# Kernel tuning notes

Hardware: AMD Instinct MI355X
Metric: run time of the kernel (lower is better)

## Reference

```python
import jax, jax.numpy as jnp
import numpy as np

B, T, D, H, S = 4, 1024, 512, 8, 16
HD = D // H
PRUNING_THRESHOLD = 0.001


def setup_inputs() -> dict:
    key = jax.random.key(0)
    ks = jax.random.split(key, 7)
    x = jax.random.normal(ks[0], (B, T, D), jnp.float32)
    qkv_w = jax.random.normal(ks[1], (3 * D, D), jnp.float32) * (1.0 / np.sqrt(D))
    out_w = jax.random.normal(ks[2], (D, D), jnp.float32) * (1.0 / np.sqrt(D))
    # diverse-ish init for centers (exact init pattern doesn't affect the math being tested)
    base_centers = jax.random.normal(ks[3], (H, S, HD), jnp.float32) * 0.3
    center_deltas = jnp.zeros((H, S, HD), jnp.float32)
    log_scales = jax.random.normal(ks[4], (H, S), jnp.float32) * 0.5 - 0.5
    log_amps = jax.random.normal(ks[5], (H, S), jnp.float32) * 1.0 - 1.5
    movement_param = jnp.asarray(0.05, jnp.float32)
    temperature = jnp.ones((1,), jnp.float32)
    return {
        "x": x, "qkv_w": qkv_w, "out_w": out_w,
        "base_centers": base_centers, "center_deltas": center_deltas,
        "log_scales": log_scales, "log_amps": log_amps,
        "movement_param": movement_param, "temperature": temperature,
    }


def reference(x, qkv_w, out_w, base_centers, center_deltas, log_scales, log_amps,
              movement_param, temperature):
    Bx, Tx, Dx = x.shape
    Hh, Ss, hd = base_centers.shape

    # qkv projection (torch Linear, no bias: y = x @ W.T)
    qkv = (x @ qkv_w.T).reshape(Bx, Tx, 3, Hh, hd)
    q, k, v = qkv[:, :, 0], qkv[:, :, 1], qkv[:, :, 2]  # [B,T,H,hd]

    # effective centers with bounded movement
    move = jax.nn.sigmoid(movement_param) * 0.2
    centers = base_centers + center_deltas * move  # [H,S,hd]

    scales = jnp.clip(jnp.exp(log_scales), 1e-4, 5.0)       # [H,S]
    amps = jnp.clip(jnp.exp(log_amps), 1e-6, 10.0)          # [H,S]
    eff_amps = amps * (amps > PRUNING_THRESHOLD).astype(amps.dtype)
    inv_var = 1.0 / (scales ** 2 + 1e-8)                     # [H,S]

    # squared distances to splat centers: [B,T,H,S]
    q_d2 = jnp.minimum(jnp.sum((q[:, :, :, None, :] - centers[None, None]) ** 2, axis=-1), 100.0)
    k_d2 = jnp.minimum(jnp.sum((k[:, :, :, None, :] - centers[None, None]) ** 2, axis=-1), 100.0)

    q_w = jnp.exp(-0.5 * q_d2 * inv_var) * eff_amps  # [B,T,H,S]
    k_w = jnp.exp(-0.5 * k_d2 * inv_var) * eff_amps  # [B,T,H,S]

    # amplitude-weighted RBF scores: [B,T,T,H]
    logits = jnp.einsum('bihs,bjhs->bijh', q_w, k_w)

    temp = jnp.clip(temperature, 0.01, 10.0)[0]
    attn = jax.nn.softmax(logits / temp + 1e-8, axis=2)  # softmax over j

    out = jnp.einsum('bijh,bjhd->bihd', attn, v).reshape(Bx, Tx, Dx)
    out = out @ out_w.T
    return (out, attn)
```

## Files before the change

### kernel.cpp

```cpp
#include <hip/hip_runtime.h>
#include <hip/hip_bf16.h>

#define B_ 4
#define T_ 1024
#define D_ 512
#define H_ 8
#define S_ 16
#define HD_ 64
#define ITS 8
#define ITW 8
#define PVI 32
#define PVJ 64

typedef short bf16x8 __attribute__((ext_vector_type(8)));
typedef float f32x4m __attribute__((ext_vector_type(4)));

__device__ __forceinline__ unsigned short f2bf(float f) {
  unsigned u = __float_as_uint(f);
  unsigned r = (u + 0x7FFFu + ((u >> 16) & 1u)) >> 16;
  return (unsigned short)r;
}
__device__ __forceinline__ float bf2f(unsigned short h) {
  return __uint_as_float((unsigned)h << 16);
}

__device__ __forceinline__ void split4(const float4 v, ushort4& h, ushort4& l) {
  h.x = f2bf(v.x); l.x = f2bf(v.x - bf2f(h.x));
  h.y = f2bf(v.y); l.y = f2bf(v.y - bf2f(h.y));
  h.z = f2bf(v.z); l.z = f2bf(v.z - bf2f(h.z));
  h.w = f2bf(v.w); l.w = f2bf(v.w - bf2f(h.w));
}

__global__ void k_params(const float* __restrict__ base_centers,
                         const float* __restrict__ center_deltas,
                         const float* __restrict__ log_scales,
                         const float* __restrict__ log_amps,
                         const float* __restrict__ movement_param,
                         const float* __restrict__ temperature,
                         float* __restrict__ centers,
                         float* __restrict__ inv_var,
                         float* __restrict__ eff_amps,
                         float* __restrict__ inv_temp) {
  int tid = blockIdx.x * blockDim.x + threadIdx.x;
  float move = (1.f / (1.f + __expf(-movement_param[0]))) * 0.2f;
  if (tid < H_ * S_ * HD_)
    centers[tid] = base_centers[tid] + center_deltas[tid] * move;
  if (tid < H_ * S_) {
    float sc = __expf(log_scales[tid]);
    sc = fminf(fmaxf(sc, 1e-4f), 5.f);
    float am = __expf(log_amps[tid]);
    am = fminf(fmaxf(am, 1e-6f), 10.f);
    inv_var[tid] = 1.f / (sc * sc + 1e-8f);
    eff_amps[tid] = (am > 0.001f) ? am : 0.f;
  }
  if (tid == 0) {
    float t = fminf(fmaxf(temperature[0], 0.01f), 10.f);
    inv_temp[0] = 1.f / t;
  }
}

template <int BN>
__global__ __launch_bounds__(256) void gemm_mfma(const float* __restrict__ A,
                                                 const float* __restrict__ Bw,
                                                 float* __restrict__ C,
                                                 int M, int N, int K) {
  static_assert(BN == 64, "staging sized for BN=64");
  constexpr int NF = BN / 16;
  const int t = threadIdx.x;
  const int lane = t & 63;
  const int wv = t >> 6;
  const int mBase = blockIdx.y * 128;
  const int n0 = blockIdx.x * BN;
  const int lr = lane & 15;
  const int kg = lane >> 4;

  __shared__ unsigned short Ash[128][64];
  __shared__ unsigned short Asl[128][64];
  __shared__ unsigned short Bsh[64][64];
  __shared__ unsigned short Bsl[64][64];

  f32x4m acc[2][NF];
#pragma unroll
  for (int i = 0; i < 2; ++i)
#pragma unroll
    for (int f = 0; f < NF; ++f) {
      f32x4m z = {0.f, 0.f, 0.f, 0.f};
      acc[i][f] = z;
    }

  for (int k0 = 0; k0 < K; k0 += 64) {
    if (k0) __syncthreads();
#pragma unroll
    for (int r2 = 0; r2 < 2; ++r2) {
      int idx = t + r2 * 256;
      int row = idx >> 3, c8 = idx & 7;
      int c8s = c8 ^ (row & 7);
      const float* src = Bw + (size_t)(n0 + row) * K + k0 + c8 * 8;
      float4 v0 = *(const float4*)(src);
      float4 v1 = *(const float4*)(src + 4);
      ushort4 h0, l0, h1, l1;
      split4(v0, h0, l0); split4(v1, h1, l1);
      *(ushort4*)&Bsh[row][c8s * 8]     = h0;
      *(ushort4*)&Bsh[row][c8s * 8 + 4] = h1;
      *(ushort4*)&Bsl[row][c8s * 8]     = l0;
      *(ushort4*)&Bsl[row][c8s * 8 + 4] = l1;
    }
#pragma unroll
    for (int r4 = 0; r4 < 4; ++r4) {
      int idx = t + r4 * 256;
      int row = idx >> 3, c8 = idx & 7;
      int c8s = c8 ^ (row & 7);
      const float* src = A + (size_t)(mBase + row) * K + k0 + c8 * 8;
      float4 v0 = *(const float4*)(src);
      float4 v1 = *(const float4*)(src + 4);
      ushort4 h0, l0, h1, l1;
      split4(v0, h0, l0); split4(v1, h1, l1);
      *(ushort4*)&Ash[row][c8s * 8]     = h0;
      *(ushort4*)&Ash[row][c8s * 8 + 4] = h1;
      *(ushort4*)&Asl[row][c8s * 8]     = l0;
      *(ushort4*)&Asl[row][c8s * 8 + 4] = l1;
    }
    __syncthreads();
#pragma unroll
    for (int S2 = 0; S2 < 2; ++S2) {
      int rowA0 = wv * 32 + lr;
      int rowA1 = rowA0 + 16;
      int slA = (S2 * 4 + kg) ^ (lr & 7);
      bf16x8 ah0 = *(const bf16x8*)&Ash[rowA0][slA * 8];
      bf16x8 ah1 = *(const bf16x8*)&Ash[rowA1][slA * 8];
      bf16x8 al0 = *(const bf16x8*)&Asl[rowA0][slA * 8];
      bf16x8 al1 = *(const bf16x8*)&Asl[rowA1][slA * 8];
#pragma unroll
      for (int f = 0; f < NF; ++f) {
        int row = f * 16 + lr;
        int sl = (S2 * 4 + kg) ^ (row & 7);
        bf16x8 vbh = *(const bf16x8*)&Bsh[row][sl * 8];
        bf16x8 vbl = *(const bf16x8*)&Bsl[row][sl * 8];
        acc[0][f] = __builtin_amdgcn_mfma_f32_16x16x32_bf16(al0, vbh, acc[0][f], 0, 0, 0);
        acc[0][f] = __builtin_amdgcn_mfma_f32_16x16x32_bf16(ah0, vbl, acc[0][f], 0, 0, 0);
        acc[0][f] = __builtin_amdgcn_mfma_f32_16x16x32_bf16(ah0, vbh, acc[0][f], 0, 0, 0);
        acc[1][f] = __builtin_amdgcn_mfma_f32_16x16x32_bf16(al1, vbh, acc[1][f], 0, 0, 0);
        acc[1][f] = __builtin_amdgcn_mfma_f32_16x16x32_bf16(ah1, vbl, acc[1][f], 0, 0, 0);
        acc[1][f] = __builtin_amdgcn_mfma_f32_16x16x32_bf16(ah1, vbh, acc[1][f], 0, 0, 0);
      }
    }
  }
  const int m0 = mBase + wv * 32;
#pragma unroll
  for (int i = 0; i < 2; ++i)
#pragma unroll
    for (int f = 0; f < NF; ++f)
#pragma unroll
      for (int r = 0; r < 4; ++r)
        C[(size_t)(m0 + i * 16 + kg * 4 + r) * N + n0 + f * 16 + lr] = acc[i][f][r];
}

template <int BN>
__global__ __launch_bounds__(128) void gemm_mfma2(const unsigned short* __restrict__ Ah,
                                                  const unsigned short* __restrict__ Al,
                                                  const float* __restrict__ Bw,
                                                  float* __restrict__ C,
                                                  int M, int N, int K) {
  static_assert(BN == 32, "staging sized for BN=32");
  constexpr int NF = BN / 16;
  const int t = threadIdx.x;
  const int lane = t & 63;
  const int wv = t >> 6;
  const int mBase = blockIdx.y * 64;
  const int n0 = blockIdx.x * BN;
  const int lr = lane & 15;
  const int kg = lane >> 4;

  __shared__ unsigned short Ash[64][64];
  __shared__ unsigned short Asl[64][64];
  __shared__ unsigned short Bsh[32][64];
  __shared__ unsigned short Bsl[32][64];

  f32x4m acc[2][NF];
#pragma unroll
  for (int i = 0; i < 2; ++i)
#pragma unroll
    for (int f = 0; f < NF; ++f) {
      f32x4m z = {0.f, 0.f, 0.f, 0.f};
      acc[i][f] = z;
    }

  for (int k0 = 0; k0 < K; k0 += 64) {
    if (k0) __syncthreads();
#pragma unroll
    for (int r2 = 0; r2 < 2; ++r2) {
      int idx = t + r2 * 128;
      int row = idx >> 3, c8 = idx & 7;
      int c8s = c8 ^ (row & 7);
      const float* src = Bw + (size_t)(n0 + row) * K + k0 + c8 * 8;
      float4 v0 = *(const float4*)(src);
      float4 v1 = *(const float4*)(src + 4);
      ushort4 h0, l0, h1, l1;
      split4(v0, h0, l0); split4(v1, h1, l1);
      *(ushort4*)&Bsh[row][c8s * 8]     = h0;
      *(ushort4*)&Bsh[row][c8s * 8 + 4] = h1;
      *(ushort4*)&Bsl[row][c8s * 8]     = l0;
      *(ushort4*)&Bsl[row][c8s * 8 + 4] = l1;
    }
#pragma unroll
    for (int r4 = 0; r4 < 4; ++r4) {
      int idx = t + r4 * 128;
      int row = idx >> 3, c8 = idx & 7;
      int c8s = c8 ^ (row & 7);
      float4 vh = *(const float4*)(Ah + (size_t)(mBase + row) * K + k0 + c8 * 8);
      float4 vl = *(const float4*)(Al + (size_t)(mBase + row) * K + k0 + c8 * 8);
      *(float4*)&Ash[row][c8s * 8] = vh;
      *(float4*)&Asl[row][c8s * 8] = vl;
    }
    __syncthreads();
#pragma unroll
    for (int S2 = 0; S2 < 2; ++S2) {
      int rowA0 = wv * 32 + lr;
      int rowA1 = rowA0 + 16;
      int slA = (S2 * 4 + kg) ^ (lr & 7);
      bf16x8 ah0 = *(const bf16x8*)&Ash[rowA0][slA * 8];
      bf16x8 ah1 = *(const bf16x8*)&Ash[rowA1][slA * 8];
      bf16x8 al0 = *(const bf16x8*)&Asl[rowA0][slA * 8];
      bf16x8 al1 = *(const bf16x8*)&Asl[rowA1][slA * 8];
#pragma unroll
      for (int f = 0; f < NF; ++f) {
        int row = f * 16 + lr;
        int sl = (S2 * 4 + kg) ^ (row & 7);
        bf16x8 vbh = *(const bf16x8*)&Bsh[row][sl * 8];
        bf16x8 vbl = *(const bf16x8*)&Bsl[row][sl * 8];
        acc[0][f] = __builtin_amdgcn_mfma_f32_16x16x32_bf16(al0, vbh, acc[0][f], 0, 0, 0);
        acc[0][f] = __builtin_amdgcn_mfma_f32_16x16x32_bf16(ah0, vbl, acc[0][f], 0, 0, 0);
        acc[0][f] = __builtin_amdgcn_mfma_f32_16x16x32_bf16(ah0, vbh, acc[0][f], 0, 0, 0);
        acc[1][f] = __builtin_amdgcn_mfma_f32_16x16x32_bf16(al1, vbh, acc[1][f], 0, 0, 0);
        acc[1][f] = __builtin_amdgcn_mfma_f32_16x16x32_bf16(ah1, vbl, acc[1][f], 0, 0, 0);
        acc[1][f] = __builtin_amdgcn_mfma_f32_16x16x32_bf16(ah1, vbh, acc[1][f], 0, 0, 0);
      }
    }
  }
  const int m0 = mBase + wv * 32;
#pragma unroll
  for (int i = 0; i < 2; ++i)
#pragma unroll
    for (int f = 0; f < NF; ++f)
#pragma unroll
      for (int r = 0; r < 4; ++r)
        C[(size_t)(m0 + i * 16 + kg * 4 + r) * N + n0 + f * 16 + lr] = acc[i][f][r];
}

__global__ __launch_bounds__(256) void k_gauss(const float* __restrict__ qkv,
                                               const float* __restrict__ centers,
                                               const float* __restrict__ inv_var,
                                               const float* __restrict__ eff_amps,
                                               const float* __restrict__ inv_temp,
                                               float* __restrict__ qw,
                                               float* __restrict__ kw) {
  int gid = blockIdx.x * blockDim.x + threadIdx.x;
  int s = gid & 7;
  int h = (gid >> 3) & 7;
  int bt = gid >> 6;
  const float* qrow = qkv + (size_t)bt * 1536 + h * 64;
  const float* krow = qrow + 512;
  const float* c0 = centers + (h * 16 + s) * 64;
  const float* c1 = c0 + 8 * 64;
  float qd0 = 0.f, kd0 = 0.f, qd1 = 0.f, kd1 = 0.f;
#pragma unroll
  for (int d = 0; d < 64; d += 4) {
    float4 qv = *(const float4*)(qrow + d);
    float4 kv = *(const float4*)(krow + d);
    float4 ca = *(const float4*)(c0 + d);
    float4 cb = *(const float4*)(c1 + d);
    float t;
    t = qv.x - ca.x; qd0 += t * t;  t = qv.y - ca.y; qd0 += t * t;
    t = qv.z - ca.z; qd0 += t * t;  t = qv.w - ca.w; qd0 += t * t;
    t = kv.x - ca.x; kd0 += t * t;  t = kv.y - ca.y; kd0 += t * t;
    t = kv.z - ca.z; kd0 += t * t;  t = kv.w - ca.w; kd0 += t * t;
    t = qv.x - cb.x; qd1 += t * t;  t = qv.y - cb.y; qd1 += t * t;
    t = qv.z - cb.z; qd1 += t * t;  t = qv.w - cb.w; qd1 += t * t;
    t = kv.x - cb.x; kd1 += t * t;  t = kv.y - cb.y; kd1 += t * t;
    t = kv.z - cb.z; kd1 += t * t;  t = kv.w - cb.w; kd1 += t * t;
  }
  qd0 = fminf(qd0, 100.f); kd0 = fminf(kd0, 100.f);
  qd1 = fminf(qd1, 100.f); kd1 = fminf(kd1, 100.f);
  float it = inv_temp[0];
  float iv0 = inv_var[h * 16 + s],     ea0 = eff_amps[h * 16 + s];
  float iv1 = inv_var[h * 16 + s + 8], ea1 = eff_amps[h * 16 + s + 8];
  size_t base = (size_t)(bt * H_ + h) * S_ + s;
  qw[base]     = __expf(-0.5f * qd0 * iv0) * ea0 * it;
  kw[base]     = __expf(-0.5f * kd0 * iv0) * ea0;
  qw[base + 8] = __expf(-0.5f * qd1 * iv1) * ea1 * it;
  kw[base + 8] = __expf(-0.5f * kd1 * iv1) * ea1;
}

__device__ __forceinline__ float dot16(const float4 q[4], const float4 k[4]) {
  return q[0].x * k[0].x + q[0].y * k[0].y + q[0].z * k[0].z + q[0].w * k[0].w +
         q[1].x * k[1].x + q[1].y * k[1].y + q[1].z * k[1].z + q[1].w * k[1].w +
         q[2].x * k[2].x + q[2].y * k[2].y + q[2].z * k[2].z + q[2].w * k[2].w +
         q[3].x * k[3].x + q[3].y * k[3].y + q[3].z * k[3].z + q[3].w * k[3].w;
}

__global__ __launch_bounds__(256, 4) void k_sv(const float* __restrict__ qw_g,
                                               const float* __restrict__ kw_g,
                                               const float* __restrict__ qkv,
                                               float* __restrict__ m_g,
                                               float* __restrict__ is_g,
                                               unsigned short* __restrict__ vth,
                                               unsigned short* __restrict__ vtl) {
  union Sm {
    float red[4][4][2][2];
    float Vl[64][68];
  };
  __shared__ Sm sm;
  const int bid = blockIdx.x;
  const int g = bid / 9;
  const int r = bid - g * 9;
  const int t = threadIdx.x;

  if (r < 8) {
    const int x = g * 8 + r;
    const int ic = x & 127;
    const int h = (x >> 7) & 7;
    const int b = x >> 10;
    const int i0 = ic * ITS;
    const int rp = t & 3;
    const int jl = t >> 2;

    float qwr[2][16], mr[2], sr[2];
#pragma unroll
    for (int e = 0; e < 2; ++e) {
      const float* qp = qw_g + (((size_t)(b * T_ + i0 + rp * 2 + e) * H_ + h) * S_);
#pragma unroll
      for (int s4 = 0; s4 < 4; ++s4) {
        float4 v = *(const float4*)(qp + s4 * 4);
        qwr[e][s4 * 4 + 0] = v.x; qwr[e][s4 * 4 + 1] = v.y;
        qwr[e][s4 * 4 + 2] = v.z; qwr[e][s4 * 4 + 3] = v.w;
      }
      mr[e] = -1e30f; sr[e] = 0.f;
    }
    for (int c = 0; c < T_ / 64; ++c) {
      int j = c * 64 + jl;
      const float* kp = kw_g + ((size_t)(b * T_ + j) * H_ + h) * S_;
      float4 k0 = *(const float4*)(kp);
      float4 k1 = *(const float4*)(kp + 4);
      float4 k2 = *(const float4*)(kp + 8);
      float4 k3 = *(const float4*)(kp + 12);
#pragma unroll
      for (int e = 0; e < 2; ++e) {
        float d = qwr[e][0] * k0.x + qwr[e][1] * k0.y + qwr[e][2] * k0.z + qwr[e][3] * k0.w +
                  qwr[e][4] * k1.x + qwr[e][5] * k1.y + qwr[e][6] * k1.z + qwr[e][7] * k1.w +
                  qwr[e][8] * k2.x + qwr[e][9] * k2.y + qwr[e][10] * k2.z + qwr[e][11] * k2.w +
                  qwr[e][12] * k3.x + qwr[e][13] * k3.y + qwr[e][14] * k3.z + qwr[e][15] * k3.w;
        float mn = fmaxf(mr[e], d);
        sr[e] = sr[e] * __expf(mr[e] - mn) + __expf(d - mn);
        mr[e] = mn;
      }
    }
#pragma unroll
    for (int o = 4; o < 64; o <<= 1) {
#pragma unroll
      for (int e = 0; e < 2; ++e) {
        float m2 = __shfl_xor(mr[e], o);
        float s2 = __shfl_xor(sr[e], o);
        float mn = fmaxf(mr[e], m2);
        sr[e] = sr[e] * __expf(mr[e] - mn) + s2 * __expf(m2 - mn);
        mr[e] = mn;
      }
    }
    int wv = t >> 6;
    if ((t & 63) < 4) {
      sm.red[wv][rp][0][0] = mr[0]; sm.red[wv][rp][0][1] = sr[0];
      sm.red[wv][rp][1][0] = mr[1]; sm.red[wv][rp][1][1] = sr[1];
    }
    __syncthreads();
    if (t < ITS) {
      int rpp = t >> 1, e = t & 1;
      float mf = sm.red[0][rpp][e][0], sf = sm.red[0][rpp][e][1];
#pragma unroll
      for (int w = 1; w < 4; ++w) {
        float m2 = sm.red[w][rpp][e][0], s2 = sm.red[w][rpp][e][1];
        float mn = fmaxf(mf, m2);
        sf = sf * __expf(mf - mn) + s2 * __expf(m2 - mn);
        mf = mn;
      }
      size_t o = (size_t)(b * H_ + h) * T_ + i0 + t;
      m_g[o] = mf;
      is_g[o] = 1.f / sf;
    }
  } else {
    const int id = g;
    const int jc = id & 15;
    const int h = (id >> 4) & 7;
    const int b = id >> 7;
    const int j0 = jc * 64;
    {
      int jj = t >> 2, dqg = t & 3;
      const float* vp = qkv + (size_t)(b * T_ + j0 + jj) * 1536 + 1024 + h * 64 + dqg * 16;
#pragma unroll
      for (int q = 0; q < 4; ++q) {
        float4 v = *(const float4*)(vp + q * 4);
        *(float4*)&sm.Vl[jj][dqg * 16 + q * 4] = v;
      }
    }
    __syncthreads();
    {
      int d = t >> 2, jg = t & 3;
      ushort4 hs[4], ls[4];
#pragma unroll
      for (int q = 0; q < 4; ++q) {
        float f0 = sm.Vl[jg * 16 + q * 4 + 0][d];
        float f1 = sm.Vl[jg * 16 + q * 4 + 1][d];
        float f2 = sm.Vl[jg * 16 + q * 4 + 2][d];
        float f3 = sm.Vl[jg * 16 + q * 4 + 3][d];
        hs[q].x = f2bf(f0); ls[q].x = f2bf(f0 - bf2f(hs[q].x));
        hs[q].y = f2bf(f1); ls[q].y = f2bf(f1 - bf2f(hs[q].y));
        hs[q].z = f2bf(f2); ls[q].z = f2bf(f2 - bf2f(hs[q].z));
        hs[q].w = f2bf(f3); ls[q].w = f2bf(f3 - bf2f(hs[q].w));
      }
      size_t off = ((size_t)(b * H_ + h) * 64 + d) * 1024 + j0 + jg * 16;
#pragma unroll
      for (int q = 0; q < 4; ++q) {
        *(ushort4*)(vth + off + q * 4) = hs[q];
        *(ushort4*)(vtl + off + q * 4) = ls[q];
      }
    }
  }
}

__global__ __launch_bounds__(256, 4) void k_attnw(const float* __restrict__ qw_g,
                                                  const float* __restrict__ kw_g,
                                                  const float* __restrict__ m_g,
                                                  const float* __restrict__ is_g,
                                                  float* __restrict__ attn) {
  const int x = blockIdx.x;
  const int jt = x & 15;
  const int it = (x >> 4) & 127;
  const int b = x >> 11;
  const int i0 = it * ITW;
  const int j0 = jt * 64;
  const int tid = threadIdx.x;

  __shared__ float qw_l[ITW][H_ * S_];
  __shared__ float msl[ITW][H_];
  __shared__ float isl[ITW][H_];
  __shared__ float tile[ITW][H_][68];

  {
    int f = tid * 4;
    int r = f >> 7, c = f & 127;
    *(float4*)&qw_l[r][c] = *(const float4*)(qw_g + ((size_t)(b * T_ + i0 + r) * 128 + c));
  }
  if (tid < 64) {
    int r = tid >> 3, hh = tid & 7;
    size_t o = (size_t)(b * H_ + hh) * T_ + i0 + r;
    msl[r][hh] = m_g[o];
    isl[r][hh] = is_g[o];
  }
  __syncthreads();

  const int h = tid >> 5;
  const int jq = tid & 31;
  const float* kw_b = kw_g + (size_t)b * T_ * (H_ * S_);
  float* attn_b = attn + (size_t)(b * T_ + i0) * (T_ * H_);

  const float* kp = kw_b + ((size_t)(j0 + jq * 2) * H_ + h) * S_;
  float4 ka[4], kb[4];
  ka[0] = *(const float4*)(kp);       ka[1] = *(const float4*)(kp + 4);
  ka[2] = *(const float4*)(kp + 8);   ka[3] = *(const float4*)(kp + 12);
  kb[0] = *(const float4*)(kp + 128); kb[1] = *(const float4*)(kp + 132);
  kb[2] = *(const float4*)(kp + 136); kb[3] = *(const float4*)(kp + 140);
#pragma unroll
  for (int r = 0; r < ITW; ++r) {
    float4 q4[4];
    q4[0] = *(const float4*)&qw_l[r][h * 16 + 0];
    q4[1] = *(const float4*)&qw_l[r][h * 16 + 4];
    q4[2] = *(const float4*)&qw_l[r][h * 16 + 8];
    q4[3] = *(const float4*)&qw_l[r][h * 16 + 12];
    float la = dot16(q4, ka);
    float lb = dot16(q4, kb);
    float mm = msl[r][h], ii = isl[r][h];
    *(float2*)&tile[r][h][jq * 2] =
        make_float2(__expf(la - mm) * ii, __expf(lb - mm) * ii);
  }
  __syncthreads();
#pragma unroll
  for (int l = 0; l < 4; ++l) {
    int f = (l * 256 + tid) * 4;
    int r = f >> 9;
    int rem = f & 511;
    int jl = rem >> 3;
    int h0 = rem & 7;
    float4 v;
    v.x = tile[r][h0 + 0][jl];
    v.y = tile[r][h0 + 1][jl];
    v.z = tile[r][h0 + 2][jl];
    v.w = tile[r][h0 + 3][jl];
    *(float4*)(attn_b + (size_t)r * (T_ * H_) + (size_t)(j0 + jl) * H_ + h0) = v;
  }
}

__global__ __launch_bounds__(256, 4) void k_pv(const float* __restrict__ qw_g,
                                               const float* __restrict__ kw_g,
                                               const float* __restrict__ m_g,
                                               const float* __restrict__ is_g,
                                               const unsigned short* __restrict__ vth,
                                               const unsigned short* __restrict__ vtl,
                                               unsigned short* __restrict__ oph,
                                               unsigned short* __restrict__ opl) {
  const int bid = blockIdx.x;
  const int xcd = bid & 7;
  const int qq = bid >> 3;
  const int p = xcd * 4 + (qq & 3);
  const int ib = qq >> 2;
  const int b = p >> 3;
  const int h = p & 7;
  const int i0 = ib * PVI;
  const int t = threadIdx.x;
  const int lane = t & 63;
  const int w = t >> 6;
  const int I = w >> 1;
  const int S = w & 1;
  const int lr = lane & 15;
  const int kg = lane >> 4;

  union Sm {
    struct {
      unsigned short Vsh[64][64];
      unsigned short Vsl[64][64];
    } v;
    float mgs[128][17];
  };
  __shared__ Sm sm;
  __shared__ float kw_sw[PVJ][16];

  const int irow = I * 16 + lr;
  float qwr[16];
  {
    const float* qp = qw_g + (((size_t)(b * T_ + i0 + irow) * H_ + h) * S_);
#pragma unroll
    for (int s4 = 0; s4 < 4; ++s4) {
      float4 v = *(const float4*)(qp + s4 * 4);
      qwr[s4 * 4 + 0] = v.x; qwr[s4 * 4 + 1] = v.y;
      qwr[s4 * 4 + 2] = v.z; qwr[s4 * 4 + 3] = v.w;
    }
  }
  float mr = m_g[(size_t)(b * H_ + h) * T_ + i0 + irow];
  float isr = is_g[(size_t)(b * H_ + h) * T_ + i0 + irow];
#pragma unroll
  for (int s = 0; s < 16; ++s) asm volatile("" : "+v"(qwr[s]));
  asm volatile("" : "+v"(mr));
  asm volatile("" : "+v"(isr));

  const unsigned short* vhp = vth + ((size_t)(b * H_ + h) * 64) * 1024;
  const unsigned short* vlp = vtl + ((size_t)(b * H_ + h) * 64) * 1024;

  f32x4m acc[4];
#pragma unroll
  for (int f = 0; f < 4; ++f) { f32x4m z = {0.f, 0.f, 0.f, 0.f}; acc[f] = z; }

  for (int jc = 0; jc < T_ / PVJ; ++jc) {
    const int j0 = jc * PVJ;
    __syncthreads();
    {
      int j = t >> 2, s4g = t & 3;
      float4 v = *(const float4*)(kw_g + (((size_t)(b * T_ + j0 + j) * H_ + h) * S_ + s4g * 4));
      int blk = s4g ^ ((j >> 3) & 3);
      *(float4*)&kw_sw[j][blk * 4] = v;
    }
#pragma unroll
    for (int u2 = 0; u2 < 2; ++u2) {
      int u = t + u2 * 256;
      int row = u >> 3, c8 = u & 7;
      int c8s = c8 ^ (row & 7);
      float4 vh = *(const float4*)(vhp + (size_t)row * 1024 + j0 + c8 * 8);
      float4 vl = *(const float4*)(vlp + (size_t)row * 1024 + j0 + c8 * 8);
      *(float4*)&sm.v.Vsh[row][c8s * 8] = vh;
      *(float4*)&sm.v.Vsl[row][c8s * 8] = vl;
    }
    __syncthreads();
    union UA { unsigned short s[8]; bf16x8 v; } AH, AL;
#pragma unroll
    for (int u = 0; u < 8; ++u) {
      int jr = S * 32 + kg * 8 + u;
      int g = (jr >> 3) & 3;
      float d = 0.f;
#pragma unroll
      for (int s4 = 0; s4 < 4; ++s4) {
        float4 kv = *(const float4*)&kw_sw[jr][(s4 ^ g) * 4];
        d += qwr[s4 * 4 + 0] * kv.x + qwr[s4 * 4 + 1] * kv.y +
             qwr[s4 * 4 + 2] * kv.z + qwr[s4 * 4 + 3] * kv.w;
      }
      float pv = __expf(d - mr) * isr;
      unsigned short hh = f2bf(pv);
      AH.s[u] = hh;
      AL.s[u] = f2bf(pv - bf2f(hh));
    }
#pragma unroll
    for (int f = 0; f < 4; ++f) {
      int row = f * 16 + lr;
      int sl = (S * 4 + kg) ^ (row & 7);
      bf16x8 BHv = *(const bf16x8*)&sm.v.Vsh[row][sl * 8];
      bf16x8 BLv = *(const bf16x8*)&sm.v.Vsl[row][sl * 8];
      acc[f] = __builtin_amdgcn_mfma_f32_16x16x32_bf16(AL.v, BHv, acc[f], 0, 0, 0);
      acc[f] = __builtin_amdgcn_mfma_f32_16x16x32_bf16(AH.v, BLv, acc[f], 0, 0, 0);
      acc[f] = __builtin_amdgcn_mfma_f32_16x16x32_bf16(AH.v, BHv, acc[f], 0, 0, 0);
    }
  }
  __syncthreads();
  if (S == 1) {
    float* dst = &sm.mgs[I * 64 + lane][0];
#pragma unroll
    for (int f = 0; f < 4; ++f)
#pragma unroll
      for (int r = 0; r < 4; ++r) dst[f * 4 + r] = acc[f][r];
  }
  __syncthreads();
  if (S == 0) {
    const float* src = &sm.mgs[I * 64 + lane][0];
#pragma unroll
    for (int f = 0; f < 4; ++f) {
#pragma unroll
      for (int r = 0; r < 4; ++r) {
        float o = acc[f][r] + src[f * 4 + r];
        unsigned short hh = f2bf(o);
        unsigned short ll = f2bf(o - bf2f(hh));
        size_t idx = (size_t)(b * T_ + i0 + I * 16 + kg * 4 + r) * D_ + h * HD_ + f * 16 + lr;
        oph[idx] = hh;
        opl[idx] = ll;
      }
    }
  }
}

extern "C" void kernel_launch(void* const* d_in, const int* in_sizes, int n_in,
                              void* d_out, int out_size, void* d_ws, size_t ws_size,
                              hipStream_t stream) {
  const float* x = (const float*)d_in[0];
  const float* qkv_w = (const float*)d_in[1];
  const float* out_w = (const float*)d_in[2];
  const float* base_c = (const float*)d_in[3];
  const float* deltas = (const float*)d_in[4];
  const float* log_sc = (const float*)d_in[5];
  const float* log_am = (const float*)d_in[6];
  const float* move_p = (const float*)d_in[7];
  const float* temp = (const float*)d_in[8];

  float* out = (float*)d_out;
  float* attn = out + (size_t)B_ * T_ * D_;

  float* ws = (float*)d_ws;
  float* qkv = ws;
  float* qw = qkv + 6291456;
  float* kw = qw + 524288;
  float* centers = kw + 524288;
  float* inv_var = centers + 8192;
  float* eff_amps = inv_var + 128;
  float* inv_temp = eff_amps + 128;
  float* m_g = inv_temp + 4;
  float* is_g = m_g + 32768;
  unsigned short* oph = (unsigned short*)(is_g + 32768);
  unsigned short* opl = oph + 2097152;
  unsigned short* vth = opl + 2097152;
  unsigned short* vtl = vth + 2097152;

  k_params<<<32, 256, 0, stream>>>(base_c, deltas, log_sc, log_am, move_p, temp,
                                   centers, inv_var, eff_amps, inv_temp);

  dim3 g1(1536 / 64, 4096 / 128);
  gemm_mfma<64><<<g1, 256, 0, stream>>>(x, qkv_w, qkv, B_ * T_, 3 * D_, D_);

  k_gauss<<<(B_ * T_ * H_ * 8) / 256, 256, 0, stream>>>(qkv, centers, inv_var,
                                                        eff_amps, inv_temp, qw, kw);
  k_sv<<<4608, 256, 0, stream>>>(qw, kw, qkv, m_g, is_g, vth, vtl);
  k_attnw<<<B_ * (T_ / ITW) * 16, 256, 0, stream>>>(qw, kw, m_g, is_g, attn);
  k_pv<<<B_ * H_ * (T_ / PVI), 256, 0, stream>>>(qw, kw, m_g, is_g, vth, vtl, oph, opl);

  dim3 g2(512 / 32, 4096 / 64);
  gemm_mfma2<32><<<g2, 128, 0, stream>>>(oph, opl, out_w, out, B_ * T_, D_, D_);
}
```

Before: 243.7 us.

## Shrink PV blocks to 16 rows and read V low bf16 half directly from global

The PV kernel now uses 128-thread blocks that each cover 16 query rows instead of 32, which doubles the grid size. The low bf16 half of V is no longer staged in shared memory; each wave loads its B-fragment straight from global memory. This cuts LDS footprint and per-block staging work, aiming for more parallelism and occupancy. The cost is that V tiles are reloaded by twice as many blocks, and the low half is read from global inside the MFMA loop, where its latency may be exposed.

```diff
diff --git a/kernel.cpp b/kernel.cpp
--- a/kernel.cpp
+++ b/kernel.cpp
@@ -9,7 +9,7 @@
 #define HD_ 64
 #define ITS 8
 #define ITW 8
-#define PVI 32
+#define PVI 16
 #define PVJ 64
 
 typedef short bf16x8 __attribute__((ext_vector_type(8)));
@@ -497,7 +497,7 @@
   }
 }
 
-__global__ __launch_bounds__(256, 4) void k_pv(const float* __restrict__ qw_g,
+__global__ __launch_bounds__(128, 4) void k_pv(const float* __restrict__ qw_g,
                                                const float* __restrict__ kw_g,
                                                const float* __restrict__ m_g,
                                                const float* __restrict__ is_g,
@@ -515,23 +515,15 @@
   const int i0 = ib * PVI;
   const int t = threadIdx.x;
   const int lane = t & 63;
-  const int w = t >> 6;
-  const int I = w >> 1;
-  const int S = w & 1;
+  const int S = t >> 6;
   const int lr = lane & 15;
   const int kg = lane >> 4;
 
-  union Sm {
-    struct {
-      unsigned short Vsh[64][64];
-      unsigned short Vsl[64][64];
-    } v;
-    float mgs[128][17];
-  };
-  __shared__ Sm sm;
+  __shared__ unsigned short Vsh[64][64];
   __shared__ float kw_sw[PVJ][16];
-
-  const int irow = I * 16 + lr;
+  __shared__ float mgs[64][17];
+
+  const int irow = lr;
   float qwr[16];
   {
     const float* qp = qw_g + (((size_t)(b * T_ + i0 + irow) * H_ + h) * S_);
@@ -559,21 +551,21 @@
   for (int jc = 0; jc < T_ / PVJ; ++jc) {
     const int j0 = jc * PVJ;
     __syncthreads();
-    {
-      int j = t >> 2, s4g = t & 3;
+#pragma unroll
+    for (int it2 = 0; it2 < 2; ++it2) {
+      int id2 = t + it2 * 128;
+      int j = id2 >> 2, s4g = id2 & 3;
       float4 v = *(const float4*)(kw_g + (((size_t)(b * T_ + j0 + j) * H_ + h) * S_ + s4g * 4));
       int blk = s4g ^ ((j >> 3) & 3);
       *(float4*)&kw_sw[j][blk * 4] = v;
     }
 #pragma unroll
-    for (int u2 = 0; u2 < 2; ++u2) {
-      int u = t + u2 * 256;
+    for (int u2 = 0; u2 < 4; ++u2) {
+      int u = t + u2 * 128;
       int row = u >> 3, c8 = u & 7;
       int c8s = c8 ^ (row & 7);
       float4 vh = *(const float4*)(vhp + (size_t)row * 1024 + j0 + c8 * 8);
-      float4 vl = *(const float4*)(vlp + (size_t)row * 1024 + j0 + c8 * 8);
-      *(float4*)&sm.v.Vsh[row][c8s * 8] = vh;
-      *(float4*)&sm.v.Vsl[row][c8s * 8] = vl;
+      *(float4*)&Vsh[row][c8s * 8] = vh;
     }
     __syncthreads();
     union UA { unsigned short s[8]; bf16x8 v; } AH, AL;
@@ -597,8 +589,8 @@
     for (int f = 0; f < 4; ++f) {
       int row = f * 16 + lr;
       int sl = (S * 4 + kg) ^ (row & 7);
-      bf16x8 BHv = *(const bf16x8*)&sm.v.Vsh[row][sl * 8];
-      bf16x8 BLv = *(const bf16x8*)&sm.v.Vsl[row][sl * 8];
+      bf16x8 BHv = *(const bf16x8*)&Vsh[row][sl * 8];
+      bf16x8 BLv = *(const bf16x8*)(vlp + (size_t)row * 1024 + j0 + S * 32 + kg * 8);
       acc[f] = __builtin_amdgcn_mfma_f32_16x16x32_bf16(AL.v, BHv, acc[f], 0, 0, 0);
       acc[f] = __builtin_amdgcn_mfma_f32_16x16x32_bf16(AH.v, BLv, acc[f], 0, 0, 0);
       acc[f] = __builtin_amdgcn_mfma_f32_16x16x32_bf16(AH.v, BHv, acc[f], 0, 0, 0);
@@ -606,7 +598,7 @@
   }
   __syncthreads();
   if (S == 1) {
-    float* dst = &sm.mgs[I * 64 + lane][0];
+    float* dst = &mgs[lane][0];
 #pragma unroll
     for (int f = 0; f < 4; ++f)
 #pragma unroll
@@ -614,7 +606,7 @@
   }
   __syncthreads();
   if (S == 0) {
-    const float* src = &sm.mgs[I * 64 + lane][0];
+    const float* src = &mgs[lane][0];
 #pragma unroll
     for (int f = 0; f < 4; ++f) {
 #pragma unroll
@@ -622,7 +614,7 @@
         float o = acc[f][r] + src[f * 4 + r];
         unsigned short hh = f2bf(o);
         unsigned short ll = f2bf(o - bf2f(hh));
-        size_t idx = (size_t)(b * T_ + i0 + I * 16 + kg * 4 + r) * D_ + h * HD_ + f * 16 + lr;
+        size_t idx = (size_t)(b * T_ + i0 + kg * 4 + r) * D_ + h * HD_ + f * 16 + lr;
         oph[idx] = hh;
         opl[idx] = ll;
       }
@@ -671,7 +663,7 @@
                                                         eff_amps, inv_temp, qw, kw);
   k_sv<<<4608, 256, 0, stream>>>(qw, kw, qkv, m_g, is_g, vth, vtl);
   k_attnw<<<B_ * (T_ / ITW) * 16, 256, 0, stream>>>(qw, kw, m_g, is_g, attn);
-  k_pv<<<B_ * H_ * (T_ / PVI), 256, 0, stream>>>(qw, kw, m_g, is_g, vth, vtl, oph, opl);
+  k_pv<<<B_ * H_ * (T_ / PVI), 128, 0, stream>>>(qw, kw, m_g, is_g, vth, vtl, oph, opl);
 
   dim3 g2(512 / 32, 4096 / 64);
   gemm_mfma2<32><<<g2, 128, 0, stream>>>(oph, opl, out_w, out, B_ * T_, D_, D_);
```

Result: no change. 239.7 us (-1.7%).
